# Performance work log

Measured on AMD Instinct MI355X. Metric: run time of the kernel, lower is better.

## Reference

```python
import jax, jax.numpy as jnp
import numpy as np

B, M, K = 32, 64, 36
DS, DX, DQ, H = 512, 128, 512, 256


def setup_inputs() -> dict:
    key = jax.random.key(0)
    ks = jax.random.split(key, 11)
    sc = lambda fan_in: 1.0 / np.sqrt(fan_in)
    return {
        "s2": jax.random.normal(ks[0], (B, M, DS), jnp.float32),
        "x0": jax.random.normal(ks[1], (B, K, DX), jnp.float32),
        "q": jax.random.normal(ks[2], (B, DQ), jnp.float32),
        # score MLP: Linear(DS+DX+DQ -> H), ReLU, Linear(H -> 1)
        "score_w1": jax.random.normal(ks[3], (DS + DX + DQ, H), jnp.float32) * sc(DS + DX + DQ),
        "score_b1": jax.random.normal(ks[4], (H,), jnp.float32) * 0.01,
        "score_w2": jax.random.normal(ks[5], (H, 1), jnp.float32) * sc(H),
        "score_b2": jax.random.normal(ks[6], (1,), jnp.float32) * 0.01,
        # h MLP: Linear(DS -> H), ReLU, Linear(H -> DX)
        "h_w1": jax.random.normal(ks[7], (DS, H), jnp.float32) * sc(DS),
        "h_b1": jax.random.normal(ks[8], (H,), jnp.float32) * 0.01,
        "h_w2": jax.random.normal(ks[9], (H, DX), jnp.float32) * sc(H),
        "h_b2": jax.random.normal(ks[10], (DX,), jnp.float32) * 0.01,
    }


def reference(s2, x0, q, score_w1, score_b1, score_w2, score_b2, h_w1, h_b1, h_w2, h_b2):
    ds = s2.shape[-1]
    dx = x0.shape[-1]
    # First score Linear over concat [s_exp, x_exp, q_exp] decomposes into
    # block matmuls (same math as Linear on the concat, no 4D concat tensor).
    w_s = score_w1[:ds]            # (DS, H)
    w_x = score_w1[ds:ds + dx]     # (DX, H)
    w_q = score_w1[ds + dx:]       # (DQ, H)
    pre_s = jnp.einsum('bmd,dh->bmh', s2, w_s)   # (b, m, H)
    pre_x = jnp.einsum('bkd,dh->bkh', x0, w_x)   # (b, k, H)
    pre_q = q @ w_q                              # (b, H)
    hidden = jax.nn.relu(pre_s[:, :, None, :] + pre_x[:, None, :, :]
                         + pre_q[:, None, None, :] + score_b1)  # (b, m, k, H)
    logits = jnp.einsum('bmkh,h->bmk', hidden, score_w2[:, 0]) + score_b2[0]
    att = jax.nn.softmax(logits, axis=1)         # softmax over m
    h_s = jax.nn.relu(s2 @ h_w1 + h_b1) @ h_w2 + h_b2  # (b, m, DX)
    agg = jnp.einsum('bmk,bmf->bkf', att, h_s)   # (b, k, DX)
    return jnp.concatenate([x0, agg], axis=-1)   # (b, k, 2*DX)
```

## Files before the change

kernel.cpp:

```cpp
#include <hip/hip_runtime.h>

#define B_  32
#define M_  64
#define K_  36
#define DS_ 512
#define DX_ 128
#define DQ_ 512
#define H_  256

#define TMA  16
#define DCH  128

__global__ __launch_bounds__(256) void kernA(
    const float* __restrict__ s2,
    const float* __restrict__ score_w1,
    const float* __restrict__ h_w1,
    const float* __restrict__ q,
    const float* __restrict__ score_b1,
    float* __restrict__ pre_s,
    float* __restrict__ ph1,
    float* __restrict__ qpre)
{
    const int t   = threadIdx.x;
    const int bid = blockIdx.x;

    if (bid >= 1024) {
        const int b = bid - 1024;
        const float* qp = q + (size_t)b * DQ_;
        const float* wq = score_w1 + (size_t)(DS_ + DX_) * H_ + t;
        float a0 = score_b1[t], a1 = 0.f, a2 = 0.f, a3 = 0.f;
        for (int d = 0; d < DQ_; d += 4) {
            const float4 q4 = *(const float4*)(qp + d);
            a0 = fmaf(q4.x, wq[(size_t)(d + 0) * H_], a0);
            a1 = fmaf(q4.y, wq[(size_t)(d + 1) * H_], a1);
            a2 = fmaf(q4.z, wq[(size_t)(d + 2) * H_], a2);
            a3 = fmaf(q4.w, wq[(size_t)(d + 3) * H_], a3);
        }
        qpre[(size_t)b * H_ + t] = (a0 + a1) + (a2 + a3);
        return;
    }

    const int tile = bid >> 3;
    const int mat  = bid & 1;
    const int dq   = (bid >> 1) & 3;

    const float* w  = (mat ? h_w1 : score_w1) + (size_t)(dq * DCH) * H_ + t;
    const float* sp = s2 + (size_t)tile * TMA * DS_ + dq * DCH;

    float acc[TMA];
    #pragma unroll
    for (int i = 0; i < TMA; ++i) acc[i] = 0.f;

    for (int d = 0; d < DCH; d += 4) {
        const float w0 = w[(size_t)(d + 0) * H_];
        const float w1 = w[(size_t)(d + 1) * H_];
        const float w2v = w[(size_t)(d + 2) * H_];
        const float w3 = w[(size_t)(d + 3) * H_];
        #pragma unroll
        for (int i = 0; i < TMA; ++i) {
            const float4 s4 = *(const float4*)(sp + (size_t)i * DS_ + d);
            acc[i] = fmaf(s4.x, w0, acc[i]);
            acc[i] = fmaf(s4.y, w1, acc[i]);
            acc[i] = fmaf(s4.z, w2v, acc[i]);
            acc[i] = fmaf(s4.w, w3, acc[i]);
        }
    }

    float* dst = (mat ? ph1 : pre_s) + (size_t)tile * TMA * H_ + t;
    #pragma unroll
    for (int i = 0; i < TMA; ++i)
        atomicAdd(dst + (size_t)i * H_, acc[i]);
}

__global__ __launch_bounds__(256) void kernC(
    const float* __restrict__ pre_s,
    const float* __restrict__ ph1,
    const float* __restrict__ qpre,
    const float* __restrict__ score_w1,
    const float* __restrict__ score_w2,
    const float* __restrict__ h_b1,
    const float* __restrict__ h_w2,
    const float* __restrict__ h_b2,
    const float* __restrict__ x0,
    float* __restrict__ out)
{
    __shared__ float cw[H_];
    __shared__ float w2s[H_];
    __shared__ float logit[M_];
    __shared__ float att[M_];
    __shared__ float part[DX_];

    const int t  = threadIdx.x;
    const int bk = blockIdx.x;
    const int b  = bk / K_;
    const float* x0p = x0 + (size_t)bk * DX_;

    w2s[t] = score_w2[t];
    {
        const float* wx = score_w1 + (size_t)DS_ * H_ + t;
        float a0 = qpre[(size_t)b * H_ + t], a1 = 0.f, a2 = 0.f, a3 = 0.f;
        for (int d = 0; d < DX_; d += 4) {
            const float4 x4 = *(const float4*)(x0p + d);
            a0 = fmaf(x4.x, wx[(size_t)(d + 0) * H_], a0);
            a1 = fmaf(x4.y, wx[(size_t)(d + 1) * H_], a1);
            a2 = fmaf(x4.z, wx[(size_t)(d + 2) * H_], a2);
            a3 = fmaf(x4.w, wx[(size_t)(d + 3) * H_], a3);
        }
        cw[t] = (a0 + a1) + (a2 + a3);
    }
    __syncthreads();

    const int wave = t >> 6, lane = t & 63;
    const float c0 = cw[lane],        c1 = cw[lane + 64],
                c2 = cw[lane + 128],  c3 = cw[lane + 192];
    const float v0 = w2s[lane],       v1 = w2s[lane + 64],
                v2 = w2s[lane + 128], v3 = w2s[lane + 192];

    const float* ps = pre_s + (size_t)b * M_ * H_;
    #pragma unroll 2
    for (int mi = 0; mi < M_ / 4 / 2; ++mi) {
        const int m0 = wave * (M_ / 4) + mi * 2;
        const float* p0 = ps + (size_t)m0 * H_;
        const float* p1 = p0 + H_;
        float pa = fmaxf(p0[lane]       + c0, 0.f) * v0
                 + fmaxf(p0[lane + 64]  + c1, 0.f) * v1
                 + fmaxf(p0[lane + 128] + c2, 0.f) * v2
                 + fmaxf(p0[lane + 192] + c3, 0.f) * v3;
        float pb = fmaxf(p1[lane]       + c0, 0.f) * v0
                 + fmaxf(p1[lane + 64]  + c1, 0.f) * v1
                 + fmaxf(p1[lane + 128] + c2, 0.f) * v2
                 + fmaxf(p1[lane + 192] + c3, 0.f) * v3;
        #pragma unroll
        for (int off = 32; off > 0; off >>= 1) {
            pa += __shfl_down(pa, off, 64);
            pb += __shfl_down(pb, off, 64);
        }
        if (lane == 0) { logit[m0] = pa; logit[m0 + 1] = pb; }
    }
    __syncthreads();

    if (wave == 0) {
        const float L = logit[lane];
        float mx = L;
        #pragma unroll
        for (int off = 32; off > 0; off >>= 1)
            mx = fmaxf(mx, __shfl_xor(mx, off, 64));
        const float e = expf(L - mx);
        float s = e;
        #pragma unroll
        for (int off = 32; off > 0; off >>= 1)
            s += __shfl_xor(s, off, 64);
        att[lane] = e / s;
    }
    __syncthreads();

    {
        const float* hp = ph1 + (size_t)b * M_ * H_ + t;
        const float b1v = h_b1[t];
        float r0 = 0.f, r1 = 0.f;
        #pragma unroll 4
        for (int m = 0; m < M_; m += 2) {
            r0 = fmaf(att[m],     fmaxf(hp[(size_t)m * H_] + b1v, 0.f), r0);
            r1 = fmaf(att[m + 1], fmaxf(hp[(size_t)(m + 1) * H_] + b1v, 0.f), r1);
        }
        cw[t] = r0 + r1;
    }
    __syncthreads();

    const int f  = t & 127;
    const int hh = t >> 7;
    const float* wp = h_w2 + (size_t)(hh * 128) * DX_ + f;
    float a0 = 0.f, a1 = 0.f, a2 = 0.f, a3 = 0.f;
    for (int h = 0; h < 128; h += 4) {
        a0 = fmaf(cw[hh * 128 + h + 0], wp[(size_t)(h + 0) * DX_], a0);
        a1 = fmaf(cw[hh * 128 + h + 1], wp[(size_t)(h + 1) * DX_], a1);
        a2 = fmaf(cw[hh * 128 + h + 2], wp[(size_t)(h + 2) * DX_], a2);
        a3 = fmaf(cw[hh * 128 + h + 3], wp[(size_t)(h + 3) * DX_], a3);
    }
    const float sum = (a0 + a1) + (a2 + a3);
    if (hh) part[f] = sum;
    __syncthreads();

    float* o = out + (size_t)bk * (2 * DX_);
    if (!hh) {
        o[DX_ + f] = sum + part[f] + h_b2[f];
    } else {
        o[f] = x0p[f];
    }
}

extern "C" void kernel_launch(void* const* d_in, const int* in_sizes, int n_in,
                              void* d_out, int out_size, void* d_ws, size_t ws_size,
                              hipStream_t stream) {
    (void)in_sizes; (void)n_in; (void)out_size; (void)ws_size;
    const float* s2       = (const float*)d_in[0];
    const float* x0       = (const float*)d_in[1];
    const float* q        = (const float*)d_in[2];
    const float* score_w1 = (const float*)d_in[3];
    const float* score_b1 = (const float*)d_in[4];
    const float* score_w2 = (const float*)d_in[5];
    const float* h_w1     = (const float*)d_in[7];
    const float* h_b1     = (const float*)d_in[8];
    const float* h_w2     = (const float*)d_in[9];
    const float* h_b2     = (const float*)d_in[10];
    float* out = (float*)d_out;

    float* ws    = (float*)d_ws;
    float* pre_s = ws;
    float* ph1   = ws + (size_t)B_ * M_ * H_;
    float* qpre  = ph1 + (size_t)B_ * M_ * H_;

    hipMemsetAsync(d_ws, 0, (size_t)2 * B_ * M_ * H_ * sizeof(float), stream);

    kernA<<<1056, 256, 0, stream>>>(s2, score_w1, h_w1, q, score_b1,
                                    pre_s, ph1, qpre);
    kernC<<<B_ * K_, 256, 0, stream>>>(pre_s, ph1, qpre, score_w1, score_w2,
                                       h_b1, h_w2, h_b2, x0, out);
}
```

Measured before the change: 132.3 us.

## Restructure pipeline: precompute h_s per row, batch four k per block, drop atomics

Splits the work into three kernels. The first computes pre_s, h1, the x projection and the q projection, reducing the inner dimension across two 256-thread halves in shared memory so no memset or atomics are needed. A new middle kernel applies the second h MLP layer to every (b,m) row once. This moves that layer ahead of the attention weighting, so the final kernel only does an attention-weighted sum over h_s. The last kernel handles four k values per block and stages the full pre_s tile for a batch in XOR-swizzled shared memory to share it across the four. The tradeoffs are an extra launch, fewer blocks in the first kernel, and 64KB of shared memory per block in the last kernel, which limits occupancy.

```diff
diff --git a/kernel.cpp b/kernel.cpp
--- a/kernel.cpp
+++ b/kernel.cpp
@@ -8,184 +8,259 @@
 #define DQ_ 512
 #define H_  256
 
-#define TMA  16
-#define DCH  128
-
-__global__ __launch_bounds__(256) void kernA(
+#define TMA 16
+
+__global__ __launch_bounds__(512) void kern1(
     const float* __restrict__ s2,
+    const float* __restrict__ x0,
+    const float* __restrict__ q,
     const float* __restrict__ score_w1,
+    const float* __restrict__ score_b1,
     const float* __restrict__ h_w1,
-    const float* __restrict__ q,
-    const float* __restrict__ score_b1,
     float* __restrict__ pre_s,
-    float* __restrict__ ph1,
+    float* __restrict__ h1,
+    float* __restrict__ px,
     float* __restrict__ qpre)
 {
+    __shared__ float comb[TMA * H_];
     const int t   = threadIdx.x;
+    const int kh  = t >> 8;
+    const int h   = t & 255;
     const int bid = blockIdx.x;
 
-    if (bid >= 1024) {
-        const int b = bid - 1024;
-        const float* qp = q + (size_t)b * DQ_;
-        const float* wq = score_w1 + (size_t)(DS_ + DX_) * H_ + t;
-        float a0 = score_b1[t], a1 = 0.f, a2 = 0.f, a3 = 0.f;
-        for (int d = 0; d < DQ_; d += 4) {
+    if (bid < 256) {
+        const int tile = bid >> 1, mat = bid & 1;
+        const float* w  = (mat ? h_w1 : score_w1) + (size_t)(kh * 256) * H_ + h;
+        const float* sp = s2 + (size_t)tile * TMA * DS_ + kh * 256;
+
+        float acc[TMA];
+        #pragma unroll
+        for (int i = 0; i < TMA; ++i) acc[i] = 0.f;
+
+        for (int d = 0; d < 256; d += 4) {
+            const float w0  = w[(size_t)(d + 0) * H_];
+            const float w1  = w[(size_t)(d + 1) * H_];
+            const float w2v = w[(size_t)(d + 2) * H_];
+            const float w3  = w[(size_t)(d + 3) * H_];
+            #pragma unroll
+            for (int i = 0; i < TMA; ++i) {
+                const float4 s4 = *(const float4*)(sp + (size_t)i * DS_ + d);
+                acc[i] = fmaf(s4.x, w0,  acc[i]);
+                acc[i] = fmaf(s4.y, w1,  acc[i]);
+                acc[i] = fmaf(s4.z, w2v, acc[i]);
+                acc[i] = fmaf(s4.w, w3,  acc[i]);
+            }
+        }
+        if (kh) {
+            #pragma unroll
+            for (int i = 0; i < TMA; ++i) comb[i * H_ + h] = acc[i];
+        }
+        __syncthreads();
+        if (!kh) {
+            float* dst = (mat ? h1 : pre_s) + (size_t)tile * TMA * H_ + h;
+            #pragma unroll
+            for (int i = 0; i < TMA; ++i)
+                dst[(size_t)i * H_] = acc[i] + comb[i * H_ + h];
+        }
+    } else if (bid < 328) {
+        const int tile = bid - 256;
+        const float* w  = score_w1 + (size_t)(DS_ + kh * 64) * H_ + h;
+        const float* sp = x0 + (size_t)tile * TMA * DX_ + kh * 64;
+
+        float acc[TMA];
+        #pragma unroll
+        for (int i = 0; i < TMA; ++i) acc[i] = 0.f;
+
+        for (int d = 0; d < 64; d += 4) {
+            const float w0  = w[(size_t)(d + 0) * H_];
+            const float w1  = w[(size_t)(d + 1) * H_];
+            const float w2v = w[(size_t)(d + 2) * H_];
+            const float w3  = w[(size_t)(d + 3) * H_];
+            #pragma unroll
+            for (int i = 0; i < TMA; ++i) {
+                const float4 s4 = *(const float4*)(sp + (size_t)i * DX_ + d);
+                acc[i] = fmaf(s4.x, w0,  acc[i]);
+                acc[i] = fmaf(s4.y, w1,  acc[i]);
+                acc[i] = fmaf(s4.z, w2v, acc[i]);
+                acc[i] = fmaf(s4.w, w3,  acc[i]);
+            }
+        }
+        if (kh) {
+            #pragma unroll
+            for (int i = 0; i < TMA; ++i) comb[i * H_ + h] = acc[i];
+        }
+        __syncthreads();
+        if (!kh) {
+            const float b1 = score_b1[h];
+            float* dst = px + (size_t)tile * TMA * H_ + h;
+            #pragma unroll
+            for (int i = 0; i < TMA; ++i)
+                dst[(size_t)i * H_] = acc[i] + comb[i * H_ + h] + b1;
+        }
+    } else {
+        const int b = bid - 328;
+        const float* qp = q + (size_t)b * DQ_ + kh * 256;
+        const float* wq = score_w1 + (size_t)(DS_ + DX_ + kh * 256) * H_ + h;
+        float a0 = 0.f, a1 = 0.f, a2 = 0.f, a3 = 0.f;
+        for (int d = 0; d < 256; d += 4) {
             const float4 q4 = *(const float4*)(qp + d);
             a0 = fmaf(q4.x, wq[(size_t)(d + 0) * H_], a0);
             a1 = fmaf(q4.y, wq[(size_t)(d + 1) * H_], a1);
             a2 = fmaf(q4.z, wq[(size_t)(d + 2) * H_], a2);
             a3 = fmaf(q4.w, wq[(size_t)(d + 3) * H_], a3);
         }
-        qpre[(size_t)b * H_ + t] = (a0 + a1) + (a2 + a3);
-        return;
-    }
-
-    const int tile = bid >> 3;
-    const int mat  = bid & 1;
-    const int dq   = (bid >> 1) & 3;
-
-    const float* w  = (mat ? h_w1 : score_w1) + (size_t)(dq * DCH) * H_ + t;
-    const float* sp = s2 + (size_t)tile * TMA * DS_ + dq * DCH;
-
-    float acc[TMA];
-    #pragma unroll
-    for (int i = 0; i < TMA; ++i) acc[i] = 0.f;
-
-    for (int d = 0; d < DCH; d += 4) {
-        const float w0 = w[(size_t)(d + 0) * H_];
-        const float w1 = w[(size_t)(d + 1) * H_];
-        const float w2v = w[(size_t)(d + 2) * H_];
-        const float w3 = w[(size_t)(d + 3) * H_];
-        #pragma unroll
-        for (int i = 0; i < TMA; ++i) {
-            const float4 s4 = *(const float4*)(sp + (size_t)i * DS_ + d);
-            acc[i] = fmaf(s4.x, w0, acc[i]);
-            acc[i] = fmaf(s4.y, w1, acc[i]);
-            acc[i] = fmaf(s4.z, w2v, acc[i]);
-            acc[i] = fmaf(s4.w, w3, acc[i]);
-        }
-    }
-
-    float* dst = (mat ? ph1 : pre_s) + (size_t)tile * TMA * H_ + t;
-    #pragma unroll
-    for (int i = 0; i < TMA; ++i)
-        atomicAdd(dst + (size_t)i * H_, acc[i]);
-}
-
-__global__ __launch_bounds__(256) void kernC(
-    const float* __restrict__ pre_s,
-    const float* __restrict__ ph1,
-    const float* __restrict__ qpre,
-    const float* __restrict__ score_w1,
-    const float* __restrict__ score_w2,
+        const float s = (a0 + a1) + (a2 + a3);
+        if (kh) comb[h] = s;
+        __syncthreads();
+        if (!kh) qpre[(size_t)b * H_ + h] = s + comb[h];
+    }
+}
+
+__global__ __launch_bounds__(256) void kern2(
+    const float* __restrict__ h1,
     const float* __restrict__ h_b1,
     const float* __restrict__ h_w2,
+    float* __restrict__ hs)
+{
+    __shared__ float A[8 * H_];
+    const int t  = threadIdx.x;
+    const int r0 = blockIdx.x * 8;
+
+    #pragma unroll
+    for (int i = 0; i < 2; ++i) {
+        const int flat = t * 4 + i * 1024;
+        const float4 v = *(const float4*)(h1 + (size_t)r0 * H_ + flat);
+        const float4 bb = *(const float4*)(h_b1 + (flat & 255));
+        float4 a;
+        a.x = fmaxf(v.x + bb.x, 0.f);
+        a.y = fmaxf(v.y + bb.y, 0.f);
+        a.z = fmaxf(v.z + bb.z, 0.f);
+        a.w = fmaxf(v.w + bb.w, 0.f);
+        *(float4*)&A[flat] = a;
+    }
+    __syncthreads();
+
+    const int f  = t & 127;
+    const int rh = t >> 7;
+    const float* wp = h_w2 + f;
+    const float* Ap = &A[rh * 4 * H_];
+
+    float a0 = 0.f, a1 = 0.f, a2 = 0.f, a3 = 0.f;
+    for (int d = 0; d < 256; d += 4) {
+        const float w0  = wp[(size_t)(d + 0) * DX_];
+        const float w1  = wp[(size_t)(d + 1) * DX_];
+        const float w2v = wp[(size_t)(d + 2) * DX_];
+        const float w3  = wp[(size_t)(d + 3) * DX_];
+        const float4 x0v = *(const float4*)&Ap[0 * H_ + d];
+        const float4 x1v = *(const float4*)&Ap[1 * H_ + d];
+        const float4 x2v = *(const float4*)&Ap[2 * H_ + d];
+        const float4 x3v = *(const float4*)&Ap[3 * H_ + d];
+        a0 = fmaf(x0v.x, w0, a0); a0 = fmaf(x0v.y, w1, a0);
+        a0 = fmaf(x0v.z, w2v, a0); a0 = fmaf(x0v.w, w3, a0);
+        a1 = fmaf(x1v.x, w0, a1); a1 = fmaf(x1v.y, w1, a1);
+        a1 = fmaf(x1v.z, w2v, a1); a1 = fmaf(x1v.w, w3, a1);
+        a2 = fmaf(x2v.x, w0, a2); a2 = fmaf(x2v.y, w1, a2);
+        a2 = fmaf(x2v.z, w2v, a2); a2 = fmaf(x2v.w, w3, a2);
+        a3 = fmaf(x3v.x, w0, a3); a3 = fmaf(x3v.y, w1, a3);
+        a3 = fmaf(x3v.z, w2v, a3); a3 = fmaf(x3v.w, w3, a3);
+    }
+    float* dst = hs + (size_t)(r0 + rh * 4) * DX_ + f;
+    dst[0 * DX_] = a0;
+    dst[1 * DX_] = a1;
+    dst[2 * DX_] = a2;
+    dst[3 * DX_] = a3;
+}
+
+__global__ __launch_bounds__(256) void kern3(
+    const float* __restrict__ pre_s,
+    const float* __restrict__ px,
+    const float* __restrict__ qpre,
+    const float* __restrict__ score_w2,
+    const float* __restrict__ hs,
     const float* __restrict__ h_b2,
     const float* __restrict__ x0,
     float* __restrict__ out)
 {
-    __shared__ float cw[H_];
-    __shared__ float w2s[H_];
-    __shared__ float logit[M_];
-    __shared__ float att[M_];
-    __shared__ float part[DX_];
-
-    const int t  = threadIdx.x;
-    const int bk = blockIdx.x;
-    const int b  = bk / K_;
-    const float* x0p = x0 + (size_t)bk * DX_;
-
-    w2s[t] = score_w2[t];
+    __shared__ float psf[M_ * H_];
+    __shared__ float cw4[4][H_];
+    __shared__ float att4[M_ * 4];
+    __shared__ float pr[4][DX_];
+
+    const int t   = threadIdx.x;
+    const int b   = blockIdx.x / 9;
+    const int k0  = (blockIdx.x % 9) * 4;
+    const int bk0 = b * K_ + k0;
+
+    const float* psrc = pre_s + (size_t)b * M_ * H_;
+    #pragma unroll
+    for (int i = 0; i < 16; ++i) {
+        const int flat = t * 4 + i * 1024;
+        const float4 v = *(const float4*)(psrc + flat);
+        const int m = flat >> 8, hh = flat & 255;
+        *(float4*)&psf[m * H_ + (hh ^ ((m & 7) << 2))] = v;
+    }
     {
-        const float* wx = score_w1 + (size_t)DS_ * H_ + t;
-        float a0 = qpre[(size_t)b * H_ + t], a1 = 0.f, a2 = 0.f, a3 = 0.f;
-        for (int d = 0; d < DX_; d += 4) {
-            const float4 x4 = *(const float4*)(x0p + d);
-            a0 = fmaf(x4.x, wx[(size_t)(d + 0) * H_], a0);
-            a1 = fmaf(x4.y, wx[(size_t)(d + 1) * H_], a1);
-            a2 = fmaf(x4.z, wx[(size_t)(d + 2) * H_], a2);
-            a3 = fmaf(x4.w, wx[(size_t)(d + 3) * H_], a3);
-        }
-        cw[t] = (a0 + a1) + (a2 + a3);
+        const float qv = qpre[(size_t)b * H_ + t];
+        #pragma unroll
+        for (int kk = 0; kk < 4; ++kk)
+            cw4[kk][t] = px[(size_t)(bk0 + kk) * H_ + t] + qv;
     }
     __syncthreads();
 
-    const int wave = t >> 6, lane = t & 63;
-    const float c0 = cw[lane],        c1 = cw[lane + 64],
-                c2 = cw[lane + 128],  c3 = cw[lane + 192];
-    const float v0 = w2s[lane],       v1 = w2s[lane + 64],
-                v2 = w2s[lane + 128], v3 = w2s[lane + 192];
-
-    const float* ps = pre_s + (size_t)b * M_ * H_;
-    #pragma unroll 2
-    for (int mi = 0; mi < M_ / 4 / 2; ++mi) {
-        const int m0 = wave * (M_ / 4) + mi * 2;
-        const float* p0 = ps + (size_t)m0 * H_;
-        const float* p1 = p0 + H_;
-        float pa = fmaxf(p0[lane]       + c0, 0.f) * v0
-                 + fmaxf(p0[lane + 64]  + c1, 0.f) * v1
-                 + fmaxf(p0[lane + 128] + c2, 0.f) * v2
-                 + fmaxf(p0[lane + 192] + c3, 0.f) * v3;
-        float pb = fmaxf(p1[lane]       + c0, 0.f) * v0
-                 + fmaxf(p1[lane + 64]  + c1, 0.f) * v1
-                 + fmaxf(p1[lane + 128] + c2, 0.f) * v2
-                 + fmaxf(p1[lane + 192] + c3, 0.f) * v3;
-        #pragma unroll
-        for (int off = 32; off > 0; off >>= 1) {
-            pa += __shfl_down(pa, off, 64);
-            pb += __shfl_down(pb, off, 64);
-        }
-        if (lane == 0) { logit[m0] = pa; logit[m0 + 1] = pb; }
-    }
-    __syncthreads();
-
-    if (wave == 0) {
-        const float L = logit[lane];
-        float mx = L;
+    {
+        const int kk = t >> 6, m = t & 63;
+        const int sw = (m & 7) << 2;
+        const float* prow = &psf[m * H_];
+        const float* crow = &cw4[kk][0];
+        float lg = 0.f;
+        for (int d = 0; d < 256; d += 4) {
+            const float4 p = *(const float4*)&prow[d ^ sw];
+            const float4 c = *(const float4*)&crow[d];
+            const float4 v = *(const float4*)(score_w2 + d);
+            lg += fmaxf(p.x + c.x, 0.f) * v.x + fmaxf(p.y + c.y, 0.f) * v.y
+                + fmaxf(p.z + c.z, 0.f) * v.z + fmaxf(p.w + c.w, 0.f) * v.w;
+        }
+        float mx = lg;
         #pragma unroll
         for (int off = 32; off > 0; off >>= 1)
             mx = fmaxf(mx, __shfl_xor(mx, off, 64));
-        const float e = expf(L - mx);
-        float s = e;
+        const float e = expf(lg - mx);
+        float sm = e;
         #pragma unroll
         for (int off = 32; off > 0; off >>= 1)
-            s += __shfl_xor(s, off, 64);
-        att[lane] = e / s;
+            sm += __shfl_xor(sm, off, 64);
+        att4[m * 4 + kk] = e / sm;
     }
     __syncthreads();
 
+    const int f = t & 127, half = t >> 7;
     {
-        const float* hp = ph1 + (size_t)b * M_ * H_ + t;
-        const float b1v = h_b1[t];
-        float r0 = 0.f, r1 = 0.f;
-        #pragma unroll 4
-        for (int m = 0; m < M_; m += 2) {
-            r0 = fmaf(att[m],     fmaxf(hp[(size_t)m * H_] + b1v, 0.f), r0);
-            r1 = fmaf(att[m + 1], fmaxf(hp[(size_t)(m + 1) * H_] + b1v, 0.f), r1);
-        }
-        cw[t] = r0 + r1;
-    }
-    __syncthreads();
-
-    const int f  = t & 127;
-    const int hh = t >> 7;
-    const float* wp = h_w2 + (size_t)(hh * 128) * DX_ + f;
-    float a0 = 0.f, a1 = 0.f, a2 = 0.f, a3 = 0.f;
-    for (int h = 0; h < 128; h += 4) {
-        a0 = fmaf(cw[hh * 128 + h + 0], wp[(size_t)(h + 0) * DX_], a0);
-        a1 = fmaf(cw[hh * 128 + h + 1], wp[(size_t)(h + 1) * DX_], a1);
-        a2 = fmaf(cw[hh * 128 + h + 2], wp[(size_t)(h + 2) * DX_], a2);
-        a3 = fmaf(cw[hh * 128 + h + 3], wp[(size_t)(h + 3) * DX_], a3);
-    }
-    const float sum = (a0 + a1) + (a2 + a3);
-    if (hh) part[f] = sum;
-    __syncthreads();
-
-    float* o = out + (size_t)bk * (2 * DX_);
-    if (!hh) {
-        o[DX_ + f] = sum + part[f] + h_b2[f];
-    } else {
-        o[f] = x0p[f];
+        const float* hsp = hs + ((size_t)b * M_ + half * 32) * DX_ + f;
+        float r0 = 0.f, r1 = 0.f, r2 = 0.f, r3 = 0.f;
+        for (int m = 0; m < 32; ++m) {
+            const float hv = hsp[(size_t)m * DX_];
+            const float4 a = *(const float4*)&att4[(half * 32 + m) * 4];
+            r0 = fmaf(a.x, hv, r0);
+            r1 = fmaf(a.y, hv, r1);
+            r2 = fmaf(a.z, hv, r2);
+            r3 = fmaf(a.w, hv, r3);
+        }
+        if (half) {
+            pr[0][f] = r0; pr[1][f] = r1; pr[2][f] = r2; pr[3][f] = r3;
+        }
+        __syncthreads();
+        if (!half) {
+            const float b2 = h_b2[f];
+            out[(size_t)(bk0 + 0) * (2 * DX_) + DX_ + f] = r0 + pr[0][f] + b2;
+            out[(size_t)(bk0 + 1) * (2 * DX_) + DX_ + f] = r1 + pr[1][f] + b2;
+            out[(size_t)(bk0 + 2) * (2 * DX_) + DX_ + f] = r2 + pr[2][f] + b2;
+            out[(size_t)(bk0 + 3) * (2 * DX_) + DX_ + f] = r3 + pr[3][f] + b2;
+        }
+    }
+    #pragma unroll
+    for (int j = 0; j < 2; ++j) {
+        const int kk = half * 2 + j;
+        out[(size_t)(bk0 + kk) * (2 * DX_) + f] = x0[(size_t)(bk0 + kk) * DX_ + f];
     }
 }
 
@@ -207,13 +282,13 @@
 
     float* ws    = (float*)d_ws;
     float* pre_s = ws;
-    float* ph1   = ws + (size_t)B_ * M_ * H_;
-    float* qpre  = ph1 + (size_t)B_ * M_ * H_;
-
-    hipMemsetAsync(d_ws, 0, (size_t)2 * B_ * M_ * H_ * sizeof(float), stream);
-
-    kernA<<<1056, 256, 0, stream>>>(s2, score_w1, h_w1, q, score_b1,
-                                    pre_s, ph1, qpre);
-    kernC<<<B_ * K_, 256, 0, stream>>>(pre_s, ph1, qpre, score_w1, score_w2,
-                                       h_b1, h_w2, h_b2, x0, out);
-}
+    float* h1    = pre_s + (size_t)B_ * M_ * H_;
+    float* px    = h1    + (size_t)B_ * M_ * H_;
+    float* qpre  = px    + (size_t)B_ * K_ * H_;
+    float* hs    = qpre  + (size_t)B_ * H_;
+
+    kern1<<<360, 512, 0, stream>>>(s2, x0, q, score_w1, score_b1, h_w1,
+                                   pre_s, h1, px, qpre);
+    kern2<<<256, 256, 0, stream>>>(h1, h_b1, h_w2, hs);
+    kern3<<<288, 256, 0, stream>>>(pre_s, px, qpre, score_w2, hs, h_b2, x0, out);
+}
```

After: 176.4 us. +33.3%, slower.
